# Performance work log

Measured on AMD Instinct MI355X. Metric: run time of the kernel, lower is better.

## Reference

```python
import jax, jax.numpy as jnp
import numpy as np

NEG_SLOPE = 0.2  # LeakyReLU slope used by PyG GATConv


def gat_conv(x, src, dst, W_src, W_dst, att_src, att_dst, bias, num_nodes):
    """Single-head PyG-style GATConv.
    x: [N, F_in]; src/dst: [E] int; W_*: [C, F_in]; att_*: [C]; bias: [C].
    """
    h_src = x @ W_src.T            # [N, C]
    h_dst = x @ W_dst.T            # [N, C]
    a_src = h_src @ att_src        # [N]
    a_dst = h_dst @ att_dst        # [N]
    e = a_src[src] + a_dst[dst]    # [E]
    e = jnp.where(e >= 0, e, NEG_SLOPE * e)  # leaky_relu
    # softmax over edges grouped by destination node
    m = jax.ops.segment_max(e, dst, num_segments=num_nodes)          # [N]
    ex = jnp.exp(e - m[dst])                                          # [E]
    denom = jax.ops.segment_sum(ex, dst, num_segments=num_nodes)      # [N]
    alpha = ex / (denom[dst] + 1e-16)                                 # [E]
    out = jax.ops.segment_sum(alpha[:, None] * h_src[src], dst,
                              num_segments=num_nodes)                 # [N, C]
    return out + bias


def setup_inputs() -> dict:
    key = jax.random.key(0)
    ks = jax.random.split(key, 16)
    N, E = 10000, 160000
    dim_in, dim_out = 4096, 20
    hid = dim_in // 4  # 1024
    x = jax.random.normal(ks[0], (N, dim_in), dtype=jnp.float32)
    edges = jax.random.randint(ks[1], (2, E), 0, N, dtype=jnp.int64)
    std = 0.01
    return {
        "x": x,
        "edges": edges,
        "W0": jax.random.normal(ks[2], (dim_out, dim_in)) * std,
        "b0": jnp.zeros((dim_out,), jnp.float32),
        "Ws1": jax.random.normal(ks[3], (hid, dim_in)) * (1.0 / np.sqrt(dim_in)),
        "Wd1": jax.random.normal(ks[4], (hid, dim_in)) * (1.0 / np.sqrt(dim_in)),
        "as1": jax.random.normal(ks[5], (hid,)) * 0.1,
        "ad1": jax.random.normal(ks[6], (hid,)) * 0.1,
        "b1": jnp.zeros((hid,), jnp.float32),
        "Ws2": jax.random.normal(ks[7], (dim_out, hid)) * (1.0 / np.sqrt(hid)),
        "Wd2": jax.random.normal(ks[8], (dim_out, hid)) * (1.0 / np.sqrt(hid)),
        "as2": jax.random.normal(ks[9], (dim_out,)) * 0.1,
        "ad2": jax.random.normal(ks[10], (dim_out,)) * 0.1,
        "b2": jnp.zeros((dim_out,), jnp.float32),
    }


def reference(x, edges, W0, b0, Ws1, Wd1, as1, ad1, b1, Ws2, Wd2, as2, ad2, b2):
    N = x.shape[0]
    # GATConv default add_self_loops=True; returned edge list includes them
    ar = jnp.arange(N, dtype=edges.dtype)
    new_edge = jnp.concatenate([edges, jnp.stack([ar, ar])], axis=1)  # [2, E+N]
    src, dst = new_edge[0], new_edge[1]

    # mil_score0: plain linear
    mil_score0 = x @ W0.T + b0                           # [N, dim_out]

    # mil_score1: two-layer GAT with ELU in between
    h = gat_conv(x, src, dst, Ws1, Wd1, as1, ad1, b1, N)  # [N, hid]
    h = jax.nn.elu(h)
    mil_score1 = gat_conv(h, src, dst, Ws2, Wd2, as2, ad2, b2, N)  # [N, dim_out]

    # softmax over proposals (dim=0) per class, fused with GAT output
    mil_score = jax.nn.softmax(mil_score0, axis=0) * mil_score1
    return (mil_score, new_edge)
```

## Files before the change

### kernel.cpp

```cpp
#include <hip/hip_runtime.h>

#define NN   10000
#define FIN  4096
#define HID  1024
#define CO   20
#define EE   160000
#define ET   170000
#define NBV  (HID + 22)

typedef __bf16 bf16x8 __attribute__((ext_vector_type(8)));
typedef float  f32x4  __attribute__((ext_vector_type(4)));

__device__ __forceinline__ float bf2f(unsigned short u) {
    unsigned int x = ((unsigned int)u) << 16;
    float f; __builtin_memcpy(&f, &x, 4); return f;
}
__device__ __forceinline__ unsigned short f2bf(float f) {
    unsigned int x; __builtin_memcpy(&x, &f, 4);
    unsigned int r = (x + 0x7fffu + ((x >> 16) & 1u)) >> 16;
    return (unsigned short)r;
}
__device__ __forceinline__ void unpack4(int2 v, float* f) {
    unsigned int a = (unsigned int)v.x, b = (unsigned int)v.y;
    f[0] = bf2f((unsigned short)(a & 0xffffu)); f[1] = bf2f((unsigned short)(a >> 16));
    f[2] = bf2f((unsigned short)(b & 0xffffu)); f[3] = bf2f((unsigned short)(b >> 16));
}
__device__ __forceinline__ int edge_at(const int* __restrict__ e, int idx, int is64) {
    return is64 ? e[2 * (size_t)idx] : e[idx];
}
__device__ __forceinline__ int4 pack8(float4 a, float4 b) {
    int4 o;
    o.x = (int)((unsigned)f2bf(a.x) | ((unsigned)f2bf(a.y) << 16));
    o.y = (int)((unsigned)f2bf(a.z) | ((unsigned)f2bf(a.w) << 16));
    o.z = (int)((unsigned)f2bf(b.x) | ((unsigned)f2bf(b.y) << 16));
    o.w = (int)((unsigned)f2bf(b.z) | ((unsigned)f2bf(b.w) << 16));
    return o;
}

__global__ void k_initA(const int* __restrict__ edg, int* __restrict__ cnt,
                        int* __restrict__ flag) {
    int i = blockIdx.x * 256 + threadIdx.x;
    if (i < NN) cnt[i] = 0;
    if (blockIdx.x == 0 && threadIdx.x < 64) {
        int v = edg[2 * threadIdx.x + 1];
        unsigned long long b = __ballot(v != 0);
        if (threadIdx.x == 0) flag[0] = (b == 0ull) ? 1 : 0;
    }
}

__global__ void k_cast(const float* __restrict__ src, unsigned short* __restrict__ dst,
                       int n8) {
    int i = blockIdx.x * 256 + threadIdx.x;
    if (i >= n8) return;
    const float4* s = (const float4*)src + (size_t)i * 2;
    *(int4*)(dst + (size_t)i * 8) = pack8(s[0], s[1]);
}

__global__ __launch_bounds__(256) void k_vecs(const float* __restrict__ Ws1,
                                              const float* __restrict__ Wd1,
                                              const float* __restrict__ as1,
                                              const float* __restrict__ ad1,
                                              float* __restrict__ partS,
                                              float* __restrict__ partD) {
    int k = blockIdx.x * 256 + threadIdx.x;
    int chunk = blockIdx.y;
    int r0 = chunk * 128;
    float s = 0.f, d = 0.f;
    for (int r = r0; r < r0 + 128; r++) {
        s += as1[r] * Ws1[(size_t)r * FIN + k];
        d += ad1[r] * Wd1[(size_t)r * FIN + k];
    }
    partS[chunk * FIN + k] = s;
    partD[chunk * FIN + k] = d;
}

__global__ void k_vred(const float* __restrict__ partS, const float* __restrict__ partD,
                       const float* __restrict__ Wd2, const float* __restrict__ ad2,
                       unsigned short* __restrict__ Bext, float* __restrict__ wd2v) {
    int k = blockIdx.x * 256 + threadIdx.x;
    if (k < FIN) {
        float s = 0.f, d = 0.f;
        for (int j = 0; j < 8; j++) { s += partS[j * FIN + k]; d += partD[j * FIN + k]; }
        Bext[(size_t)(HID + CO) * FIN + k]     = f2bf(s);
        Bext[(size_t)(HID + CO + 1) * FIN + k] = f2bf(d);
    }
    if (k < HID) {
        float d2 = 0.f;
        for (int r = 0; r < CO; r++) d2 += ad2[r] * Wd2[(size_t)r * HID + k];
        wd2v[k] = d2;
    }
}

__global__ void k_bext(const float* __restrict__ Ws1, const float* __restrict__ W0,
                       unsigned short* __restrict__ Bext) {
    int i = blockIdx.x * 256 + threadIdx.x;
    if (i >= (HID + CO) * (FIN / 8)) return;
    int row = i >> 9;
    int col = (i & 511) * 8;
    const float* src = (row < HID) ? Ws1 + (size_t)row * FIN
                                   : W0 + (size_t)(row - HID) * FIN;
    const float4* s = (const float4*)(src + col);
    *(int4*)(Bext + (size_t)row * FIN + col) = pack8(s[0], s[1]);
}

#define GBM 128
#define GBN 128
#define GBK 32
#define NMT ((NN + GBM - 1) / GBM)
#define NNT ((NBV + GBN - 1) / GBN)
#define NWG (NMT * NNT)

__global__ __launch_bounds__(256) void k_gemm_ext(
    const unsigned short* __restrict__ A, const unsigned short* __restrict__ B,
    unsigned short* __restrict__ H1, float* __restrict__ ext, int M) {
    __shared__ __bf16 As[2][GBM * GBK];
    __shared__ __bf16 Bs[2][GBN * GBK];
    int bid = blockIdx.x;
    int q = NWG >> 3, r = NWG & 7;
    int xcd = bid & 7, idx = bid >> 3;
    int swz = (xcd < r ? xcd * (q + 1) : r * (q + 1) + (xcd - r) * q) + idx;
    int mt = swz / NNT;
    int nt = swz - mt * NNT;
    int m0 = mt * GBM;
    int n0 = nt * GBN;
    int tid = threadIdx.x;
    int lane = tid & 63, wave = tid >> 6;
    int wm = (wave >> 1) * 64, wn = (wave & 1) * 64;
    int lrow = lane & 15, lk8 = (lane >> 4) * 8;

    int srow = lane >> 2;
    int scol = (lane & 3) * 8;
    int arow = wave * 32;
    int gmA0 = m0 + arow + srow;      if (gmA0 >= M) gmA0 = M - 1;
    int gmA1 = m0 + arow + 16 + srow; if (gmA1 >= M) gmA1 = M - 1;
    int gnB0 = n0 + arow + srow;      if (gnB0 >= NBV) gnB0 = NBV - 1;
    int gnB1 = n0 + arow + 16 + srow; if (gnB1 >= NBV) gnB1 = NBV - 1;
    const unsigned short* pA0 = A + (size_t)gmA0 * FIN + scol;
    const unsigned short* pA1 = A + (size_t)gmA1 * FIN + scol;
    const unsigned short* pB0 = B + (size_t)gnB0 * FIN + scol;
    const unsigned short* pB1 = B + (size_t)gnB1 * FIN + scol;

    f32x4 acc[4][4];
#pragma unroll
    for (int r2 = 0; r2 < 4; r2++)
#pragma unroll
        for (int c = 0; c < 4; c++) acc[r2][c] = (f32x4){0.f, 0.f, 0.f, 0.f};

    auto stage = [&](int buf, int k0) {
        __builtin_amdgcn_global_load_lds(
            (const __attribute__((address_space(1))) void*)(pA0 + k0),
            (__attribute__((address_space(3))) void*)&As[buf][arow * GBK], 16, 0, 0);
        __builtin_amdgcn_global_load_lds(
            (const __attribute__((address_space(1))) void*)(pA1 + k0),
            (__attribute__((address_space(3))) void*)&As[buf][(arow + 16) * GBK], 16, 0, 0);
        __builtin_amdgcn_global_load_lds(
            (const __attribute__((address_space(1))) void*)(pB0 + k0),
            (__attribute__((address_space(3))) void*)&Bs[buf][arow * GBK], 16, 0, 0);
        __builtin_amdgcn_global_load_lds(
            (const __attribute__((address_space(1))) void*)(pB1 + k0),
            (__attribute__((address_space(3))) void*)&Bs[buf][(arow + 16) * GBK], 16, 0, 0);
    };

    stage(0, 0);
    int cur = 0;
    for (int k0 = 0; k0 < FIN; k0 += GBK) {
        __syncthreads();
        if (k0 + GBK < FIN) stage(cur ^ 1, k0 + GBK);
        bf16x8 af[4], bfr[4];
#pragma unroll
        for (int r2 = 0; r2 < 4; r2++)
            af[r2] = *(const bf16x8*)(&As[cur][(wm + r2 * 16 + lrow) * GBK + lk8]);
#pragma unroll
        for (int c = 0; c < 4; c++)
            bfr[c] = *(const bf16x8*)(&Bs[cur][(wn + c * 16 + lrow) * GBK + lk8]);
#pragma unroll
        for (int r2 = 0; r2 < 4; r2++)
#pragma unroll
            for (int c = 0; c < 4; c++)
                acc[r2][c] = __builtin_amdgcn_mfma_f32_16x16x32_bf16(af[r2], bfr[c], acc[r2][c], 0, 0, 0);
        cur ^= 1;
    }
    int orow = (lane >> 4) * 4, ocol = lane & 15;
#pragma unroll
    for (int r2 = 0; r2 < 4; r2++)
#pragma unroll
        for (int c = 0; c < 4; c++)
#pragma unroll
            for (int i = 0; i < 4; i++) {
                int m = m0 + wm + r2 * 16 + orow + i;
                int n = n0 + wn + c * 16 + ocol;
                if (m < M) {
                    float v = acc[r2][c][i];
                    if (n < HID)      H1[(size_t)m * HID + n] = f2bf(v);
                    else if (n < NBV) ext[(size_t)(n - HID) * NN + m] = v;
                }
            }
}

__global__ void k_count(const int* __restrict__ edges, const int* __restrict__ flag,
                        int* __restrict__ cnt) {
    int k = blockIdx.x * 256 + threadIdx.x;
    if (k >= ET) return;
    int is64 = flag[0];
    int d = (k < EE) ? edge_at(edges, EE + k, is64) : (k - EE);
    if ((unsigned)d < NN) atomicAdd(&cnt[d], 1);
}

__global__ __launch_bounds__(1024) void k_scan(const int* __restrict__ cnt,
                                               int* __restrict__ offs,
                                               int* __restrict__ cursor) {
    int t = threadIdx.x, lane = t & 63, wv = t >> 6;
    int base = t * 10;
    int c[10]; int tot = 0;
    if (base < NN) {
#pragma unroll
        for (int j = 0; j < 10; j++) { c[j] = cnt[base + j]; tot += c[j]; }
    }
    int incl = tot;
#pragma unroll
    for (int o = 1; o < 64; o <<= 1) {
        int v = __shfl_up(incl, o, 64);
        if (lane >= o) incl += v;
    }
    __shared__ int wsum[16];
    if (lane == 63) wsum[wv] = incl;
    __syncthreads();
    if (t < 16) {
        int v = wsum[t];
        int inc2 = v;
#pragma unroll
        for (int o = 1; o < 16; o <<= 1) {
            int u = __shfl_up(inc2, o, 64);
            if (t >= o) inc2 += u;
        }
        wsum[t] = inc2 - v;
    }
    __syncthreads();
    int excl = incl - tot + wsum[wv];
    if (base < NN) {
        int run = excl;
#pragma unroll
        for (int j = 0; j < 10; j++) {
            cursor[base + j] = run;
            run += c[j];
            offs[base + j + 1] = run;
        }
    }
    if (t == 0) offs[0] = 0;
}

__global__ void k_scatter(const int* __restrict__ edges, const int* __restrict__ flag,
                          int* __restrict__ cursor, int* __restrict__ csr_src) {
    int k = blockIdx.x * 256 + threadIdx.x;
    if (k >= ET) return;
    int is64 = flag[0];
    int s, d;
    if (k < EE) { s = edge_at(edges, k, is64); d = edge_at(edges, EE + k, is64); }
    else        { s = d = k - EE; }
    if ((unsigned)d >= NN) return;
    if ((unsigned)s >= NN) s = 0;
    int pos = atomicAdd(&cursor[d], 1);
    csr_src[pos] = s;
}

__global__ __launch_bounds__(64) void k_alpha(const int* __restrict__ offs,
                                              const int* __restrict__ csr,
                                              const float* __restrict__ a_src,
                                              const float* __restrict__ a_dst,
                                              float* __restrict__ alpha) {
    int n = blockIdx.x, lane = threadIdx.x;
    int b = offs[n], deg = offs[n + 1] - b;
    float ad = a_dst[n];
    float mymax = -INFINITY;
    for (int j = lane; j < deg; j += 64) {
        float v = a_src[csr[b + j]] + ad;
        v = (v >= 0.f) ? v : 0.2f * v;
        mymax = fmaxf(mymax, v);
    }
    for (int o = 32; o; o >>= 1) mymax = fmaxf(mymax, __shfl_xor(mymax, o, 64));
    float mysum = 0.f;
    for (int j = lane; j < deg; j += 64) {
        float v = a_src[csr[b + j]] + ad;
        v = (v >= 0.f) ? v : 0.2f * v;
        mysum += expf(v - mymax);
    }
    for (int o = 32; o; o >>= 1) mysum += __shfl_xor(mysum, o, 64);
    float inv = 1.0f / (mysum + 1e-16f);
    for (int j = lane; j < deg; j += 64) {
        float v = a_src[csr[b + j]] + ad;
        v = (v >= 0.f) ? v : 0.2f * v;
        alpha[b + j] = expf(v - mymax) * inv;
    }
}

__global__ __launch_bounds__(256) void k_agg1f(
    const int* __restrict__ offs, const int* __restrict__ csr,
    const float* __restrict__ alpha, const unsigned short* __restrict__ H1,
    const float* __restrict__ b1, const float* __restrict__ Ws2,
    const float* __restrict__ wd2v, const float* __restrict__ as2,
    float* __restrict__ H2, float* __restrict__ a_src2, float* __restrict__ a_dst2) {
    int n = blockIdx.x, t = threadIdx.x, lane = t & 63, wv = t >> 6;
    int b = offs[n], deg = offs[n + 1] - b;
    float acc[4] = {0.f, 0.f, 0.f, 0.f};
    for (int j = 0; j < deg; j++) {
        int s = csr[b + j];
        float w = alpha[b + j];
        float f[4]; unpack4(*(const int2*)(H1 + (size_t)s * HID + t * 4), f);
        acc[0] += w * f[0]; acc[1] += w * f[1];
        acc[2] += w * f[2]; acc[3] += w * f[3];
    }
    float4 bb = *(const float4*)(b1 + t * 4);
    float xf[4];
    xf[0] = acc[0] + bb.x; xf[1] = acc[1] + bb.y;
    xf[2] = acc[2] + bb.z; xf[3] = acc[3] + bb.w;
#pragma unroll
    for (int i = 0; i < 4; i++)
        xf[i] = (xf[i] > 0.f) ? xf[i] : (expf(xf[i]) - 1.f);
    float part[21];
#pragma unroll
    for (int c = 0; c < CO; c++) {
        float4 wf = *(const float4*)(Ws2 + (size_t)c * HID + t * 4);
        part[c] = xf[0]*wf.x + xf[1]*wf.y + xf[2]*wf.z + xf[3]*wf.w;
    }
    {
        float4 w = *(const float4*)(wd2v + t * 4);
        part[20] = xf[0]*w.x + xf[1]*w.y + xf[2]*w.z + xf[3]*w.w;
    }
    __shared__ float red[21][4];
    __shared__ float dv[21];
#pragma unroll
    for (int v = 0; v < 21; v++) {
        float s = part[v];
        for (int o = 32; o; o >>= 1) s += __shfl_down(s, o, 64);
        if (lane == 0) red[v][wv] = s;
    }
    __syncthreads();
    if (t < 21) {
        float s = red[t][0] + red[t][1] + red[t][2] + red[t][3];
        dv[t] = s;
        if (t < CO) H2[(size_t)n * CO + t] = s;
        else        a_dst2[n] = s;
    }
    __syncthreads();
    if (t == 0) {
        float a = 0.f;
        for (int c = 0; c < CO; c++) a += dv[c] * as2[c];
        a_src2[n] = a;
    }
}

__global__ __launch_bounds__(64) void k_agg2(const int* __restrict__ offs,
                                             const int* __restrict__ csr,
                                             const float* __restrict__ alpha,
                                             const float* __restrict__ H2,
                                             const float* __restrict__ b2,
                                             float* __restrict__ ms1T) {
    int n = blockIdx.x, t = threadIdx.x;
    if (t >= CO) return;
    int b = offs[n], deg = offs[n + 1] - b;
    float acc = 0.f;
    for (int j = 0; j < deg; j++)
        acc += alpha[b + j] * H2[(size_t)csr[b + j] * CO + t];
    ms1T[(size_t)t * NN + n] = acc + b2[t];
}

__global__ __launch_bounds__(256) void k_fstat(const float* __restrict__ ext,
                                               float* __restrict__ gmax,
                                               float* __restrict__ ginv) {
    int c = blockIdx.x, t = threadIdx.x, lane = t & 63, wv = t >> 6;
    const float* row = ext + (size_t)c * NN;
    __shared__ float r4[4];
    __shared__ float bv;
    float m = -INFINITY;
    for (int n = t; n < NN; n += 256) m = fmaxf(m, row[n]);
    for (int o = 32; o; o >>= 1) m = fmaxf(m, __shfl_xor(m, o, 64));
    if (lane == 0) r4[wv] = m;
    __syncthreads();
    if (t == 0) bv = fmaxf(fmaxf(r4[0], r4[1]), fmaxf(r4[2], r4[3]));
    __syncthreads();
    float gm = bv;
    __syncthreads();
    float s = 0.f;
    for (int n = t; n < NN; n += 256) s += expf(row[n] - gm);
    for (int o = 32; o; o >>= 1) s += __shfl_xor(s, o, 64);
    if (lane == 0) r4[wv] = s;
    __syncthreads();
    if (t == 0) { gmax[c] = gm; ginv[c] = 1.0f / (r4[0] + r4[1] + r4[2] + r4[3]); }
}

__global__ __launch_bounds__(256) void k_fout(const float* __restrict__ ext,
                                              const float* __restrict__ ms1T,
                                              const float* __restrict__ gmax,
                                              const float* __restrict__ ginv,
                                              const int* __restrict__ edges,
                                              const int* __restrict__ flag,
                                              float* __restrict__ out) {
    int g = blockIdx.x * 256 + threadIdx.x;
    if (g < NN) {
        float o[CO];
#pragma unroll
        for (int c = 0; c < CO; c++)
            o[c] = expf(ext[(size_t)c * NN + g] - gmax[c]) * ginv[c] * ms1T[(size_t)c * NN + g];
#pragma unroll
        for (int c = 0; c < CO; c += 4) {
            float4 v; v.x = o[c]; v.y = o[c + 1]; v.z = o[c + 2]; v.w = o[c + 3];
            *(float4*)(out + (size_t)g * CO + c) = v;
        }
    }
    if (g < ET) {
        int is64 = flag[0];
        int s, d;
        if (g < EE) { s = edge_at(edges, g, is64); d = edge_at(edges, EE + g, is64); }
        else        { s = d = g - EE; }
        out[NN * CO + g]      = bf2f(f2bf((float)s));
        out[NN * CO + ET + g] = bf2f(f2bf((float)d));
    }
}

extern "C" void kernel_launch(void* const* d_in, const int* in_sizes, int n_in,
                              void* d_out, int out_size, void* d_ws, size_t ws_size,
                              hipStream_t stream) {
    const float* x   = (const float*)d_in[0];
    const int*   edg = (const int*)d_in[1];
    const float* W0  = (const float*)d_in[2];
    const float* Ws1 = (const float*)d_in[4];
    const float* Wd1 = (const float*)d_in[5];
    const float* as1 = (const float*)d_in[6];
    const float* ad1 = (const float*)d_in[7];
    const float* b1  = (const float*)d_in[8];
    const float* Ws2 = (const float*)d_in[9];
    const float* Wd2 = (const float*)d_in[10];
    const float* as2 = (const float*)d_in[11];
    const float* ad2 = (const float*)d_in[12];
    const float* b2  = (const float*)d_in[13];
    float* out = (float*)d_out;

    char* p = (char*)d_ws;
    auto alloc = [&](size_t bytes) -> char* {
        char* r = p; p += (bytes + 511) & ~((size_t)511); return r;
    };
    unsigned short* xb   = (unsigned short*)alloc((size_t)NN * FIN * 2);
    unsigned short* Bext = (unsigned short*)alloc((size_t)NBV * FIN * 2);
    unsigned short* H1   = (unsigned short*)alloc((size_t)NN * HID * 2);
    float* ext    = (float*)alloc((size_t)22 * NN * 4);
    float* partS  = (float*)alloc((size_t)8 * FIN * 4);
    float* partD  = (float*)alloc((size_t)8 * FIN * 4);
    float* wd2v   = (float*)alloc(HID * 4);
    float* H2     = (float*)alloc((size_t)NN * CO * 4);
    float* ms1T   = (float*)alloc((size_t)CO * NN * 4);
    float* a_src2 = (float*)alloc(NN * 4);
    float* a_dst2 = (float*)alloc(NN * 4);
    float* alpha  = (float*)alloc((size_t)ET * 4);
    int* csr_src  = (int*)alloc((size_t)ET * 4);
    int* cnt      = (int*)alloc(NN * 4);
    int* offs     = (int*)alloc((NN + 1) * 4);
    int* cursor   = (int*)alloc(NN * 4);
    int* eflag    = (int*)alloc(64);
    float* gmax   = (float*)alloc(CO * 4);
    float* ginv   = (float*)alloc(CO * 4);

    k_initA<<<(NN + 255) / 256, 256, 0, stream>>>(edg, cnt, eflag);
    k_cast<<<(NN * FIN / 8 + 255) / 256, 256, 0, stream>>>(x, xb, NN * FIN / 8);
    dim3 vg(FIN / 256, 8);
    k_vecs<<<vg, 256, 0, stream>>>(Ws1, Wd1, as1, ad1, partS, partD);
    k_vred<<<FIN / 256, 256, 0, stream>>>(partS, partD, Wd2, ad2, Bext, wd2v);
    k_bext<<<((HID + CO) * (FIN / 8) + 255) / 256, 256, 0, stream>>>(Ws1, W0, Bext);
    k_gemm_ext<<<NWG, 256, 0, stream>>>(xb, Bext, H1, ext, NN);
    k_count<<<(ET + 255) / 256, 256, 0, stream>>>(edg, eflag, cnt);
    k_scan<<<1, 1024, 0, stream>>>(cnt, offs, cursor);
    k_scatter<<<(ET + 255) / 256, 256, 0, stream>>>(edg, eflag, cursor, csr_src);
    k_fstat<<<CO, 256, 0, stream>>>(ext, gmax, ginv);
    k_alpha<<<NN, 64, 0, stream>>>(offs, csr_src, ext + 20 * NN, ext + 21 * NN, alpha);
    k_agg1f<<<NN, 256, 0, stream>>>(offs, csr_src, alpha, H1, b1, Ws2, wd2v, as2,
                                    H2, a_src2, a_dst2);
    k_alpha<<<NN, 64, 0, stream>>>(offs, csr_src, a_src2, a_dst2, alpha);
    k_agg2<<<NN, 64, 0, stream>>>(offs, csr_src, alpha, H2, b2, ms1T);
    k_fout<<<(ET + 255) / 256, 256, 0, stream>>>(ext, ms1T, gmax, ginv, edg, eflag, out);
}
```

Measured before the change: 622.8 us.

## Enlarge GEMM tiles to 256x256 with triple-buffered LDS pipeline

Rewrites the main bf16 MFMA GEMM to use 256x256x32 tiles with 512 threads per block, giving each wave a 128x64 output patch. Global-to-LDS staging is now triple-buffered with explicit vmcnt waits and one barrier per k-step, and s_setprio is raised around the MFMA burst. The aim is more data reuse per LDS load and better overlap of loads with compute. In exchange only 200 workgroups are launched for 256 CUs, and the last N tile is mostly padding, so the larger tiles may leave CUs idle and waste work.

```diff
diff --git a/kernel.cpp b/kernel.cpp
--- a/kernel.cpp
+++ b/kernel.cpp
@@ -103,94 +103,104 @@
     *(int4*)(Bext + (size_t)row * FIN + col) = pack8(s[0], s[1]);
 }
 
-#define GBM 128
-#define GBN 128
-#define GBK 32
-#define NMT ((NN + GBM - 1) / GBM)
-#define NNT ((NBV + GBN - 1) / GBN)
+#define TBM 256
+#define TBN 256
+#define TBK 32
+#define TNT (FIN / TBK)
+#define NMT ((NN + TBM - 1) / TBM)
+#define NNT ((NBV + TBN - 1) / TBN)
 #define NWG (NMT * NNT)
 
-__global__ __launch_bounds__(256) void k_gemm_ext(
+#define GLD16(src, dst) __builtin_amdgcn_global_load_lds(                         \
+    (const __attribute__((address_space(1))) void*)(src),                         \
+    (__attribute__((address_space(3))) void*)(dst), 16, 0, 0)
+
+__global__ __launch_bounds__(512, 2) void k_gemm_ext(
     const unsigned short* __restrict__ A, const unsigned short* __restrict__ B,
     unsigned short* __restrict__ H1, float* __restrict__ ext, int M) {
-    __shared__ __bf16 As[2][GBM * GBK];
-    __shared__ __bf16 Bs[2][GBN * GBK];
+    __shared__ __bf16 AS[3][TBM * TBK];
+    __shared__ __bf16 BS[3][TBN * TBK];
+
     int bid = blockIdx.x;
     int q = NWG >> 3, r = NWG & 7;
     int xcd = bid & 7, idx = bid >> 3;
     int swz = (xcd < r ? xcd * (q + 1) : r * (q + 1) + (xcd - r) * q) + idx;
-    int mt = swz / NNT;
-    int nt = swz - mt * NNT;
-    int m0 = mt * GBM;
-    int n0 = nt * GBN;
-    int tid = threadIdx.x;
-    int lane = tid & 63, wave = tid >> 6;
-    int wm = (wave >> 1) * 64, wn = (wave & 1) * 64;
+    int mt = swz / NNT, nt = swz - mt * NNT;
+    int m0 = mt * TBM, n0 = nt * TBN;
+
+    int tid = threadIdx.x, lane = tid & 63, wave = tid >> 6;
+    int wm = (wave >> 2) * 128, wn = (wave & 3) * 64;
     int lrow = lane & 15, lk8 = (lane >> 4) * 8;
 
-    int srow = lane >> 2;
-    int scol = (lane & 3) * 8;
-    int arow = wave * 32;
-    int gmA0 = m0 + arow + srow;      if (gmA0 >= M) gmA0 = M - 1;
-    int gmA1 = m0 + arow + 16 + srow; if (gmA1 >= M) gmA1 = M - 1;
-    int gnB0 = n0 + arow + srow;      if (gnB0 >= NBV) gnB0 = NBV - 1;
-    int gnB1 = n0 + arow + 16 + srow; if (gnB1 >= NBV) gnB1 = NBV - 1;
-    const unsigned short* pA0 = A + (size_t)gmA0 * FIN + scol;
-    const unsigned short* pA1 = A + (size_t)gmA1 * FIN + scol;
-    const unsigned short* pB0 = B + (size_t)gnB0 * FIN + scol;
-    const unsigned short* pB1 = B + (size_t)gnB1 * FIN + scol;
-
-    f32x4 acc[4][4];
-#pragma unroll
-    for (int r2 = 0; r2 < 4; r2++)
-#pragma unroll
-        for (int c = 0; c < 4; c++) acc[r2][c] = (f32x4){0.f, 0.f, 0.f, 0.f};
-
-    auto stage = [&](int buf, int k0) {
-        __builtin_amdgcn_global_load_lds(
-            (const __attribute__((address_space(1))) void*)(pA0 + k0),
-            (__attribute__((address_space(3))) void*)&As[buf][arow * GBK], 16, 0, 0);
-        __builtin_amdgcn_global_load_lds(
-            (const __attribute__((address_space(1))) void*)(pA1 + k0),
-            (__attribute__((address_space(3))) void*)&As[buf][(arow + 16) * GBK], 16, 0, 0);
-        __builtin_amdgcn_global_load_lds(
-            (const __attribute__((address_space(1))) void*)(pB0 + k0),
-            (__attribute__((address_space(3))) void*)&Bs[buf][arow * GBK], 16, 0, 0);
-        __builtin_amdgcn_global_load_lds(
-            (const __attribute__((address_space(1))) void*)(pB1 + k0),
-            (__attribute__((address_space(3))) void*)&Bs[buf][(arow + 16) * GBK], 16, 0, 0);
+    int c0 = tid, c1 = tid + 512;
+    int ar0 = m0 + (c0 >> 2); if (ar0 >= M) ar0 = M - 1;
+    int ar1 = m0 + (c1 >> 2); if (ar1 >= M) ar1 = M - 1;
+    int br0 = n0 + (c0 >> 2); if (br0 >= NBV) br0 = NBV - 1;
+    int br1 = n0 + (c1 >> 2); if (br1 >= NBV) br1 = NBV - 1;
+    const unsigned short* pA0 = A + (size_t)ar0 * FIN + (c0 & 3) * 8;
+    const unsigned short* pA1 = A + (size_t)ar1 * FIN + (c1 & 3) * 8;
+    const unsigned short* pB0 = B + (size_t)br0 * FIN + (c0 & 3) * 8;
+    const unsigned short* pB1 = B + (size_t)br1 * FIN + (c1 & 3) * 8;
+    int d0 = (wave * 64) * 8;
+    int d1 = (wave * 64 + 512) * 8;
+
+    f32x4 acc[8][4];
+#pragma unroll
+    for (int mf = 0; mf < 8; mf++)
+#pragma unroll
+        for (int nf = 0; nf < 4; nf++) acc[mf][nf] = (f32x4){0.f, 0.f, 0.f, 0.f};
+
+    auto stage = [&](int t) {
+        int s = t % 3;
+        size_t ko = (size_t)t * TBK;
+        GLD16(pA0 + ko, &AS[s][d0]);
+        GLD16(pA1 + ko, &AS[s][d1]);
+        GLD16(pB0 + ko, &BS[s][d0]);
+        GLD16(pB1 + ko, &BS[s][d1]);
     };
 
-    stage(0, 0);
-    int cur = 0;
-    for (int k0 = 0; k0 < FIN; k0 += GBK) {
-        __syncthreads();
-        if (k0 + GBK < FIN) stage(cur ^ 1, k0 + GBK);
-        bf16x8 af[4], bfr[4];
-#pragma unroll
-        for (int r2 = 0; r2 < 4; r2++)
-            af[r2] = *(const bf16x8*)(&As[cur][(wm + r2 * 16 + lrow) * GBK + lk8]);
-#pragma unroll
-        for (int c = 0; c < 4; c++)
-            bfr[c] = *(const bf16x8*)(&Bs[cur][(wn + c * 16 + lrow) * GBK + lk8]);
-#pragma unroll
-        for (int r2 = 0; r2 < 4; r2++)
-#pragma unroll
-            for (int c = 0; c < 4; c++)
-                acc[r2][c] = __builtin_amdgcn_mfma_f32_16x16x32_bf16(af[r2], bfr[c], acc[r2][c], 0, 0, 0);
-        cur ^= 1;
-    }
+    stage(0);
+    stage(1);
+
+    auto compute_tile = [&](int t) {
+        int s = t % 3;
+        bf16x8 af[8], bf[4];
+#pragma unroll
+        for (int mf = 0; mf < 8; mf++)
+            af[mf] = *(const bf16x8*)(&AS[s][(wm + mf * 16 + lrow) * TBK + lk8]);
+#pragma unroll
+        for (int nf = 0; nf < 4; nf++)
+            bf[nf] = *(const bf16x8*)(&BS[s][(wn + nf * 16 + lrow) * TBK + lk8]);
+        __builtin_amdgcn_s_setprio(1);
+#pragma unroll
+        for (int mf = 0; mf < 8; mf++)
+#pragma unroll
+            for (int nf = 0; nf < 4; nf++)
+                acc[mf][nf] = __builtin_amdgcn_mfma_f32_16x16x32_bf16(af[mf], bf[nf], acc[mf][nf], 0, 0, 0);
+        __builtin_amdgcn_s_setprio(0);
+    };
+
+    for (int t = 0; t < TNT - 1; ++t) {
+        asm volatile("s_waitcnt vmcnt(4)" ::: "memory");
+        __builtin_amdgcn_s_barrier();
+        if (t + 2 < TNT) stage(t + 2);
+        compute_tile(t);
+    }
+    asm volatile("s_waitcnt vmcnt(0)" ::: "memory");
+    __builtin_amdgcn_s_barrier();
+    compute_tile(TNT - 1);
+
     int orow = (lane >> 4) * 4, ocol = lane & 15;
 #pragma unroll
-    for (int r2 = 0; r2 < 4; r2++)
-#pragma unroll
-        for (int c = 0; c < 4; c++)
+    for (int mf = 0; mf < 8; mf++)
+#pragma unroll
+        for (int nf = 0; nf < 4; nf++)
 #pragma unroll
             for (int i = 0; i < 4; i++) {
-                int m = m0 + wm + r2 * 16 + orow + i;
-                int n = n0 + wn + c * 16 + ocol;
+                int m = m0 + wm + mf * 16 + orow + i;
+                int n = n0 + wn + nf * 16 + ocol;
                 if (m < M) {
-                    float v = acc[r2][c][i];
+                    float v = acc[mf][nf][i];
                     if (n < HID)      H1[(size_t)m * HID + n] = f2bf(v);
                     else if (n < NBV) ext[(size_t)(n - HID) * NN + m] = v;
                 }
@@ -465,7 +475,7 @@
     k_vecs<<<vg, 256, 0, stream>>>(Ws1, Wd1, as1, ad1, partS, partD);
     k_vred<<<FIN / 256, 256, 0, stream>>>(partS, partD, Wd2, ad2, Bext, wd2v);
     k_bext<<<((HID + CO) * (FIN / 8) + 255) / 256, 256, 0, stream>>>(Ws1, W0, Bext);
-    k_gemm_ext<<<NWG, 256, 0, stream>>>(xb, Bext, H1, ext, NN);
+    k_gemm_ext<<<NWG, 512, 0, stream>>>(xb, Bext, H1, ext, NN);
     k_count<<<(ET + 255) / 256, 256, 0, stream>>>(edg, eflag, cnt);
     k_scan<<<1, 1024, 0, stream>>>(cnt, offs, cursor);
     k_scatter<<<(ET + 255) / 256, 256, 0, stream>>>(edg, eflag, cursor, csr_src);
```

After: 655.3 us. 5.2% more time.

## Fuse edge-softmax into aggregation kernels and merge small prep launches

Applied to the files above, without the earlier changes.

Computes the per-destination edge softmax weights inside the aggregation kernels and caches them in shared memory, which removes both k_alpha launches and the global alpha buffer round trip. It also merges the init work into the cast kernel, bext and vecs into one prep kernel, and count and fstat into one kernel, cutting launch count. The edge scores are now computed three times per node (max, sum, weights), which adds gather work. Most of the time is still in the large GEMM, so the expected gain is modest.

```diff
diff --git a/kernel.cpp b/kernel.cpp
--- a/kernel.cpp
+++ b/kernel.cpp
@@ -37,41 +37,50 @@
     return o;
 }
 
-__global__ void k_initA(const int* __restrict__ edg, int* __restrict__ cnt,
-                        int* __restrict__ flag) {
+__global__ void k_cast(const float* __restrict__ src, unsigned short* __restrict__ dst,
+                       const int* __restrict__ edg, int* __restrict__ cnt,
+                       int* __restrict__ flag) {
     int i = blockIdx.x * 256 + threadIdx.x;
-    if (i < NN) cnt[i] = 0;
-    if (blockIdx.x == 0 && threadIdx.x < 64) {
-        int v = edg[2 * threadIdx.x + 1];
-        unsigned long long b = __ballot(v != 0);
-        if (threadIdx.x == 0) flag[0] = (b == 0ull) ? 1 : 0;
-    }
-}
-
-__global__ void k_cast(const float* __restrict__ src, unsigned short* __restrict__ dst,
-                       int n8) {
-    int i = blockIdx.x * 256 + threadIdx.x;
-    if (i >= n8) return;
     const float4* s = (const float4*)src + (size_t)i * 2;
     *(int4*)(dst + (size_t)i * 8) = pack8(s[0], s[1]);
-}
-
-__global__ __launch_bounds__(256) void k_vecs(const float* __restrict__ Ws1,
+    if (i < NN) cnt[i] = 0;
+    if (i < 64) {
+        int v = edg[2 * i + 1];
+        unsigned long long bm = __ballot(v != 0);
+        if (i == 0) flag[0] = (bm == 0ull) ? 1 : 0;
+    }
+}
+
+#define BEXTB 2088
+__global__ __launch_bounds__(256) void k_prep(const float* __restrict__ Ws1,
                                               const float* __restrict__ Wd1,
+                                              const float* __restrict__ W0,
                                               const float* __restrict__ as1,
                                               const float* __restrict__ ad1,
+                                              unsigned short* __restrict__ Bext,
                                               float* __restrict__ partS,
                                               float* __restrict__ partD) {
-    int k = blockIdx.x * 256 + threadIdx.x;
-    int chunk = blockIdx.y;
-    int r0 = chunk * 128;
-    float s = 0.f, d = 0.f;
-    for (int r = r0; r < r0 + 128; r++) {
-        s += as1[r] * Ws1[(size_t)r * FIN + k];
-        d += ad1[r] * Wd1[(size_t)r * FIN + k];
-    }
-    partS[chunk * FIN + k] = s;
-    partD[chunk * FIN + k] = d;
+    if (blockIdx.x < BEXTB) {
+        int i = blockIdx.x * 256 + threadIdx.x;
+        int row = i >> 9;
+        int col = (i & 511) * 8;
+        const float* src = (row < HID) ? Ws1 + (size_t)row * FIN
+                                       : W0 + (size_t)(row - HID) * FIN;
+        const float4* s = (const float4*)(src + col);
+        *(int4*)(Bext + (size_t)row * FIN + col) = pack8(s[0], s[1]);
+    } else {
+        int bx = blockIdx.x - BEXTB;
+        int k = (bx & 15) * 256 + threadIdx.x;
+        int chunk = bx >> 4;
+        int r0 = chunk * 128;
+        float s = 0.f, d = 0.f;
+        for (int r = r0; r < r0 + 128; r++) {
+            s += as1[r] * Ws1[(size_t)r * FIN + k];
+            d += ad1[r] * Wd1[(size_t)r * FIN + k];
+        }
+        partS[chunk * FIN + k] = s;
+        partD[chunk * FIN + k] = d;
+    }
 }
 
 __global__ void k_vred(const float* __restrict__ partS, const float* __restrict__ partD,
@@ -89,18 +98,6 @@
         for (int r = 0; r < CO; r++) d2 += ad2[r] * Wd2[(size_t)r * HID + k];
         wd2v[k] = d2;
     }
-}
-
-__global__ void k_bext(const float* __restrict__ Ws1, const float* __restrict__ W0,
-                       unsigned short* __restrict__ Bext) {
-    int i = blockIdx.x * 256 + threadIdx.x;
-    if (i >= (HID + CO) * (FIN / 8)) return;
-    int row = i >> 9;
-    int col = (i & 511) * 8;
-    const float* src = (row < HID) ? Ws1 + (size_t)row * FIN
-                                   : W0 + (size_t)(row - HID) * FIN;
-    const float4* s = (const float4*)(src + col);
-    *(int4*)(Bext + (size_t)row * FIN + col) = pack8(s[0], s[1]);
 }
 
 #define GBM 128
@@ -197,13 +194,40 @@
             }
 }
 
-__global__ void k_count(const int* __restrict__ edges, const int* __restrict__ flag,
-                        int* __restrict__ cnt) {
-    int k = blockIdx.x * 256 + threadIdx.x;
-    if (k >= ET) return;
-    int is64 = flag[0];
-    int d = (k < EE) ? edge_at(edges, EE + k, is64) : (k - EE);
-    if ((unsigned)d < NN) atomicAdd(&cnt[d], 1);
+#define CNTB 665
+__global__ __launch_bounds__(256) void k_cfs(const int* __restrict__ edges,
+                                             const int* __restrict__ flag,
+                                             int* __restrict__ cnt,
+                                             const float* __restrict__ ext,
+                                             float* __restrict__ gmax,
+                                             float* __restrict__ ginv) {
+    if (blockIdx.x < CNTB) {
+        int k = blockIdx.x * 256 + threadIdx.x;
+        if (k >= ET) return;
+        int is64 = flag[0];
+        int d = (k < EE) ? edge_at(edges, EE + k, is64) : (k - EE);
+        if ((unsigned)d < NN) atomicAdd(&cnt[d], 1);
+    } else {
+        int c = blockIdx.x - CNTB, t = threadIdx.x, lane = t & 63, wv = t >> 6;
+        const float* row = ext + (size_t)c * NN;
+        __shared__ float r4[4];
+        __shared__ float bv;
+        float m = -INFINITY;
+        for (int n = t; n < NN; n += 256) m = fmaxf(m, row[n]);
+        for (int o = 32; o; o >>= 1) m = fmaxf(m, __shfl_xor(m, o, 64));
+        if (lane == 0) r4[wv] = m;
+        __syncthreads();
+        if (t == 0) bv = fmaxf(fmaxf(r4[0], r4[1]), fmaxf(r4[2], r4[3]));
+        __syncthreads();
+        float gm = bv;
+        __syncthreads();
+        float s = 0.f;
+        for (int n = t; n < NN; n += 256) s += expf(row[n] - gm);
+        for (int o = 32; o; o >>= 1) s += __shfl_xor(s, o, 64);
+        if (lane == 0) r4[wv] = s;
+        __syncthreads();
+        if (t == 0) { gmax[c] = gm; ginv[c] = 1.0f / (r4[0] + r4[1] + r4[2] + r4[3]); }
+    }
 }
 
 __global__ __launch_bounds__(1024) void k_scan(const int* __restrict__ cnt,
@@ -263,11 +287,104 @@
     csr_src[pos] = s;
 }
 
-__global__ __launch_bounds__(64) void k_alpha(const int* __restrict__ offs,
-                                              const int* __restrict__ csr,
-                                              const float* __restrict__ a_src,
-                                              const float* __restrict__ a_dst,
-                                              float* __restrict__ alpha) {
+__global__ __launch_bounds__(256) void k_agg1f(
+    const int* __restrict__ offs, const int* __restrict__ csr,
+    const float* __restrict__ a_src, const float* __restrict__ a_dst,
+    const unsigned short* __restrict__ H1,
+    const float* __restrict__ b1, const float* __restrict__ Ws2,
+    const float* __restrict__ wd2v, const float* __restrict__ as2,
+    float* __restrict__ H2, float* __restrict__ a_src2, float* __restrict__ a_dst2) {
+    int n = blockIdx.x, t = threadIdx.x, lane = t & 63, wv = t >> 6;
+    int b = offs[n], deg = offs[n + 1] - b;
+    float ad = a_dst[n];
+    __shared__ float r4[4];
+    __shared__ float acache[1024];
+    float mymax = -INFINITY;
+    for (int j = t; j < deg; j += 256) {
+        float v = a_src[csr[b + j]] + ad;
+        v = (v >= 0.f) ? v : 0.2f * v;
+        mymax = fmaxf(mymax, v);
+    }
+    for (int o = 32; o; o >>= 1) mymax = fmaxf(mymax, __shfl_xor(mymax, o, 64));
+    if (lane == 0) r4[wv] = mymax;
+    __syncthreads();
+    float gm = fmaxf(fmaxf(r4[0], r4[1]), fmaxf(r4[2], r4[3]));
+    __syncthreads();
+    float mysum = 0.f;
+    for (int j = t; j < deg; j += 256) {
+        float v = a_src[csr[b + j]] + ad;
+        v = (v >= 0.f) ? v : 0.2f * v;
+        mysum += expf(v - gm);
+    }
+    for (int o = 32; o; o >>= 1) mysum += __shfl_xor(mysum, o, 64);
+    if (lane == 0) r4[wv] = mysum;
+    __syncthreads();
+    float inv = 1.0f / (r4[0] + r4[1] + r4[2] + r4[3] + 1e-16f);
+    float acc[4] = {0.f, 0.f, 0.f, 0.f};
+    for (int base = 0; base < deg; base += 1024) {
+        int lim = deg - base; if (lim > 1024) lim = 1024;
+        __syncthreads();
+        for (int j = t; j < lim; j += 256) {
+            float v = a_src[csr[b + base + j]] + ad;
+            v = (v >= 0.f) ? v : 0.2f * v;
+            acache[j] = expf(v - gm) * inv;
+        }
+        __syncthreads();
+        for (int j = 0; j < lim; j++) {
+            int s = csr[b + base + j];
+            float w = acache[j];
+            float f[4]; unpack4(*(const int2*)(H1 + (size_t)s * HID + t * 4), f);
+            acc[0] += w * f[0]; acc[1] += w * f[1];
+            acc[2] += w * f[2]; acc[3] += w * f[3];
+        }
+    }
+    float4 bb = *(const float4*)(b1 + t * 4);
+    float xf[4];
+    xf[0] = acc[0] + bb.x; xf[1] = acc[1] + bb.y;
+    xf[2] = acc[2] + bb.z; xf[3] = acc[3] + bb.w;
+#pragma unroll
+    for (int i = 0; i < 4; i++)
+        xf[i] = (xf[i] > 0.f) ? xf[i] : (expf(xf[i]) - 1.f);
+    float part[21];
+#pragma unroll
+    for (int c = 0; c < CO; c++) {
+        float4 wf = *(const float4*)(Ws2 + (size_t)c * HID + t * 4);
+        part[c] = xf[0]*wf.x + xf[1]*wf.y + xf[2]*wf.z + xf[3]*wf.w;
+    }
+    {
+        float4 w = *(const float4*)(wd2v + t * 4);
+        part[20] = xf[0]*w.x + xf[1]*w.y + xf[2]*w.z + xf[3]*w.w;
+    }
+    __shared__ float red[21][4];
+    __shared__ float dv[21];
+#pragma unroll
+    for (int v = 0; v < 21; v++) {
+        float s = part[v];
+        for (int o = 32; o; o >>= 1) s += __shfl_down(s, o, 64);
+        if (lane == 0) red[v][wv] = s;
+    }
+    __syncthreads();
+    if (t < 21) {
+        float s = red[t][0] + red[t][1] + red[t][2] + red[t][3];
+        dv[t] = s;
+        if (t < CO) H2[(size_t)n * CO + t] = s;
+        else        a_dst2[n] = s;
+    }
+    __syncthreads();
+    if (t == 0) {
+        float a = 0.f;
+        for (int c = 0; c < CO; c++) a += dv[c] * as2[c];
+        a_src2[n] = a;
+    }
+}
+
+__global__ __launch_bounds__(64) void k_agg2(const int* __restrict__ offs,
+                                             const int* __restrict__ csr,
+                                             const float* __restrict__ a_src,
+                                             const float* __restrict__ a_dst,
+                                             const float* __restrict__ H2,
+                                             const float* __restrict__ b2,
+                                             float* __restrict__ ms1T) {
     int n = blockIdx.x, lane = threadIdx.x;
     int b = offs[n], deg = offs[n + 1] - b;
     float ad = a_dst[n];
@@ -286,106 +403,22 @@
     }
     for (int o = 32; o; o >>= 1) mysum += __shfl_xor(mysum, o, 64);
     float inv = 1.0f / (mysum + 1e-16f);
-    for (int j = lane; j < deg; j += 64) {
-        float v = a_src[csr[b + j]] + ad;
-        v = (v >= 0.f) ? v : 0.2f * v;
-        alpha[b + j] = expf(v - mymax) * inv;
-    }
-}
-
-__global__ __launch_bounds__(256) void k_agg1f(
-    const int* __restrict__ offs, const int* __restrict__ csr,
-    const float* __restrict__ alpha, const unsigned short* __restrict__ H1,
-    const float* __restrict__ b1, const float* __restrict__ Ws2,
-    const float* __restrict__ wd2v, const float* __restrict__ as2,
-    float* __restrict__ H2, float* __restrict__ a_src2, float* __restrict__ a_dst2) {
-    int n = blockIdx.x, t = threadIdx.x, lane = t & 63, wv = t >> 6;
-    int b = offs[n], deg = offs[n + 1] - b;
-    float acc[4] = {0.f, 0.f, 0.f, 0.f};
-    for (int j = 0; j < deg; j++) {
-        int s = csr[b + j];
-        float w = alpha[b + j];
-        float f[4]; unpack4(*(const int2*)(H1 + (size_t)s * HID + t * 4), f);
-        acc[0] += w * f[0]; acc[1] += w * f[1];
-        acc[2] += w * f[2]; acc[3] += w * f[3];
-    }
-    float4 bb = *(const float4*)(b1 + t * 4);
-    float xf[4];
-    xf[0] = acc[0] + bb.x; xf[1] = acc[1] + bb.y;
-    xf[2] = acc[2] + bb.z; xf[3] = acc[3] + bb.w;
-#pragma unroll
-    for (int i = 0; i < 4; i++)
-        xf[i] = (xf[i] > 0.f) ? xf[i] : (expf(xf[i]) - 1.f);
-    float part[21];
-#pragma unroll
-    for (int c = 0; c < CO; c++) {
-        float4 wf = *(const float4*)(Ws2 + (size_t)c * HID + t * 4);
-        part[c] = xf[0]*wf.x + xf[1]*wf.y + xf[2]*wf.z + xf[3]*wf.w;
-    }
-    {
-        float4 w = *(const float4*)(wd2v + t * 4);
-        part[20] = xf[0]*w.x + xf[1]*w.y + xf[2]*w.z + xf[3]*w.w;
-    }
-    __shared__ float red[21][4];
-    __shared__ float dv[21];
-#pragma unroll
-    for (int v = 0; v < 21; v++) {
-        float s = part[v];
-        for (int o = 32; o; o >>= 1) s += __shfl_down(s, o, 64);
-        if (lane == 0) red[v][wv] = s;
-    }
-    __syncthreads();
-    if (t < 21) {
-        float s = red[t][0] + red[t][1] + red[t][2] + red[t][3];
-        dv[t] = s;
-        if (t < CO) H2[(size_t)n * CO + t] = s;
-        else        a_dst2[n] = s;
-    }
-    __syncthreads();
-    if (t == 0) {
-        float a = 0.f;
-        for (int c = 0; c < CO; c++) a += dv[c] * as2[c];
-        a_src2[n] = a;
-    }
-}
-
-__global__ __launch_bounds__(64) void k_agg2(const int* __restrict__ offs,
-                                             const int* __restrict__ csr,
-                                             const float* __restrict__ alpha,
-                                             const float* __restrict__ H2,
-                                             const float* __restrict__ b2,
-                                             float* __restrict__ ms1T) {
-    int n = blockIdx.x, t = threadIdx.x;
-    if (t >= CO) return;
-    int b = offs[n], deg = offs[n + 1] - b;
+    __shared__ float acache[256];
     float acc = 0.f;
-    for (int j = 0; j < deg; j++)
-        acc += alpha[b + j] * H2[(size_t)csr[b + j] * CO + t];
-    ms1T[(size_t)t * NN + n] = acc + b2[t];
-}
-
-__global__ __launch_bounds__(256) void k_fstat(const float* __restrict__ ext,
-                                               float* __restrict__ gmax,
-                                               float* __restrict__ ginv) {
-    int c = blockIdx.x, t = threadIdx.x, lane = t & 63, wv = t >> 6;
-    const float* row = ext + (size_t)c * NN;
-    __shared__ float r4[4];
-    __shared__ float bv;
-    float m = -INFINITY;
-    for (int n = t; n < NN; n += 256) m = fmaxf(m, row[n]);
-    for (int o = 32; o; o >>= 1) m = fmaxf(m, __shfl_xor(m, o, 64));
-    if (lane == 0) r4[wv] = m;
-    __syncthreads();
-    if (t == 0) bv = fmaxf(fmaxf(r4[0], r4[1]), fmaxf(r4[2], r4[3]));
-    __syncthreads();
-    float gm = bv;
-    __syncthreads();
-    float s = 0.f;
-    for (int n = t; n < NN; n += 256) s += expf(row[n] - gm);
-    for (int o = 32; o; o >>= 1) s += __shfl_xor(s, o, 64);
-    if (lane == 0) r4[wv] = s;
-    __syncthreads();
-    if (t == 0) { gmax[c] = gm; ginv[c] = 1.0f / (r4[0] + r4[1] + r4[2] + r4[3]); }
+    for (int base = 0; base < deg; base += 256) {
+        int lim = deg - base; if (lim > 256) lim = 256;
+        __syncthreads();
+        for (int j = lane; j < lim; j += 64) {
+            float v = a_src[csr[b + base + j]] + ad;
+            v = (v >= 0.f) ? v : 0.2f * v;
+            acache[j] = expf(v - mymax) * inv;
+        }
+        __syncthreads();
+        if (lane < CO)
+            for (int j = 0; j < lim; j++)
+                acc += acache[j] * H2[(size_t)csr[b + base + j] * CO + lane];
+    }
+    if (lane < CO) ms1T[(size_t)lane * NN + n] = acc + b2[lane];
 }
 
 __global__ __launch_bounds__(256) void k_fout(const float* __restrict__ ext,
@@ -450,7 +483,6 @@
     float* ms1T   = (float*)alloc((size_t)CO * NN * 4);
     float* a_src2 = (float*)alloc(NN * 4);
     float* a_dst2 = (float*)alloc(NN * 4);
-    float* alpha  = (float*)alloc((size_t)ET * 4);
     int* csr_src  = (int*)alloc((size_t)ET * 4);
     int* cnt      = (int*)alloc(NN * 4);
     int* offs     = (int*)alloc((NN + 1) * 4);
@@ -459,21 +491,15 @@
     float* gmax   = (float*)alloc(CO * 4);
     float* ginv   = (float*)alloc(CO * 4);
 
-    k_initA<<<(NN + 255) / 256, 256, 0, stream>>>(edg, cnt, eflag);
-    k_cast<<<(NN * FIN / 8 + 255) / 256, 256, 0, stream>>>(x, xb, NN * FIN / 8);
-    dim3 vg(FIN / 256, 8);
-    k_vecs<<<vg, 256, 0, stream>>>(Ws1, Wd1, as1, ad1, partS, partD);
+    k_cast<<<NN * FIN / 8 / 256, 256, 0, stream>>>(x, xb, edg, cnt, eflag);
+    k_prep<<<BEXTB + 128, 256, 0, stream>>>(Ws1, Wd1, W0, as1, ad1, Bext, partS, partD);
     k_vred<<<FIN / 256, 256, 0, stream>>>(partS, partD, Wd2, ad2, Bext, wd2v);
-    k_bext<<<((HID + CO) * (FIN / 8) + 255) / 256, 256, 0, stream>>>(Ws1, W0, Bext);
     k_gemm_ext<<<NWG, 256, 0, stream>>>(xb, Bext, H1, ext, NN);
-    k_count<<<(ET + 255) / 256, 256, 0, stream>>>(edg, eflag, cnt);
+    k_cfs<<<CNTB + CO, 256, 0, stream>>>(edg, eflag, cnt, ext, gmax, ginv);
     k_scan<<<1, 1024, 0, stream>>>(cnt, offs, cursor);
     k_scatter<<<(ET + 255) / 256, 256, 0, stream>>>(edg, eflag, cursor, csr_src);
-    k_fstat<<<CO, 256, 0, stream>>>(ext, gmax, ginv);
-    k_alpha<<<NN, 64, 0, stream>>>(offs, csr_src, ext + 20 * NN, ext + 21 * NN, alpha);
-    k_agg1f<<<NN, 256, 0, stream>>>(offs, csr_src, alpha, H1, b1, Ws2, wd2v, as2,
-                                    H2, a_src2, a_dst2);
-    k_alpha<<<NN, 64, 0, stream>>>(offs, csr_src, a_src2, a_dst2, alpha);
-    k_agg2<<<NN, 64, 0, stream>>>(offs, csr_src, alpha, H2, b2, ms1T);
+    k_agg1f<<<NN, 256, 0, stream>>>(offs, csr_src, ext + 20 * NN, ext + 21 * NN, H1,
+                                    b1, Ws2, wd2v, as2, H2, a_src2, a_dst2);
+    k_agg2<<<NN, 64, 0, stream>>>(offs, csr_src, a_src2, a_dst2, H2, b2, ms1T);
     k_fout<<<(ET + 255) / 256, 256, 0, stream>>>(ext, ms1T, gmax, ginv, edg, eflag, out);
 }
```

Result: faster. 601.6 us (-3.4%).
